# Performance work log

Hardware: AMD Instinct MI355X
Metric: run time of the kernel (lower is better)

The kernel has to match this reference:

```python
import jax, jax.numpy as jnp
import numpy as np

H = 256; NH = 4; DH = H // NH
NT, NS, NV = 4096, 2048, 1024
E1, E2, E3 = 65536, 16384, 32768
LN_EPS = 1e-5


def setup_inputs() -> dict:
    key = jax.random.key(0)
    ks = jax.random.split(key, 40)
    def nrm(i, shape):
        return jax.random.normal(ks[i], shape, jnp.float32) * 0.05
    inp = {
        "x_term": jax.random.normal(ks[0], (NT, H), jnp.float32),
        "x_symbol": jax.random.normal(ks[1], (NS, H), jnp.float32),
        "x_var": jax.random.normal(ks[2], (NV, H), jnp.float32),
        "ha_src": jax.random.randint(ks[3], (E1,), 0, NT),
        "ha_dst": jax.random.randint(ks[4], (E1,), 0, NT),
        "so_src": jax.random.randint(ks[5], (E2,), 0, NT),
        "so_dst": jax.random.randint(ks[6], (E2,), 0, NS),
        "vo_src": jax.random.randint(ks[7], (E3,), 0, NV),
        "vo_dst": jax.random.randint(ks[8], (E3,), 0, NT),
        # SAGEConv params for the 4 term-destination relations
        "Wl_rha": nrm(9, (H, H)),  "bl_rha": nrm(10, (H,)), "Wr_rha": nrm(11, (H, H)),
        "Wl_ha":  nrm(12, (H, H)), "bl_ha":  nrm(13, (H,)), "Wr_ha":  nrm(14, (H, H)),
        "Wl_rsym": nrm(15, (H, H)), "bl_rsym": nrm(16, (H,)), "Wr_rsym": nrm(17, (H, H)),
        "Wl_var": nrm(18, (H, H)), "bl_var": nrm(19, (H,)), "Wr_var": nrm(20, (H, H)),
        "ln_g": jnp.ones((H,), jnp.float32),
        "ln_b": jnp.zeros((H,), jnp.float32),
        "in_proj_w": nrm(21, (3 * H, H)),
        "in_proj_b": nrm(22, (3 * H,)),
        "out_proj_w": nrm(23, (H, H)),
        "out_proj_b": nrm(24, (H,)),
        "post_w": nrm(25, (H, H)),
        "post_b": nrm(26, (H,)),
    }
    return inp


def _sage(x_src, x_dst, src, dst, Wl, bl, Wr, num_dst):
    # PyG SAGEConv: lin_l(mean_j x_src[j]) + lin_r(x_dst)
    msg = x_src[src]                                            # [E, H] gather
    s = jax.ops.segment_sum(msg, dst, num_segments=num_dst)     # [N_dst, H] scatter-add
    cnt = jax.ops.segment_sum(jnp.ones((src.shape[0],), x_src.dtype), dst,
                              num_segments=num_dst)
    agg = s / jnp.maximum(cnt, 1.0)[:, None]
    return agg @ Wl.T + bl + x_dst @ Wr.T


def _layernorm(x, g, b):
    mu = jnp.mean(x, axis=-1, keepdims=True)
    var = jnp.mean(jnp.square(x - mu), axis=-1, keepdims=True)
    return (x - mu) * jax.lax.rsqrt(var + LN_EPS) * g + b


def _mha(x, in_w, in_b, out_w, out_b):
    # torch MultiheadAttention (eval, batch=1, self-attention)
    qkv = x @ in_w.T + in_b                       # [N, 3H]
    q, k, v = jnp.split(qkv, 3, axis=-1)
    def heads(t):
        return t.reshape(-1, NH, DH).transpose(1, 0, 2)  # [NH, N, DH]
    q, k, v = heads(q), heads(k), heads(v)
    scores = jnp.einsum("hqd,hkd->hqk", q, k) / np.sqrt(DH).astype(np.float32)
    a = jax.nn.softmax(scores, axis=-1)
    o = jnp.einsum("hqk,hkd->hqd", a, v)          # [NH, N, DH]
    o = o.transpose(1, 0, 2).reshape(-1, H)
    return o @ out_w.T + out_b


def reference(x_term, x_symbol, x_var,
              ha_src, ha_dst, so_src, so_dst, vo_src, vo_dst,
              Wl_rha, bl_rha, Wr_rha, Wl_ha, bl_ha, Wr_ha,
              Wl_rsym, bl_rsym, Wr_rsym, Wl_var, bl_var, Wr_var,
              ln_g, ln_b, in_proj_w, in_proj_b, out_proj_w, out_proj_b,
              post_w, post_b):
    nt = x_term.shape[0]
    # HeteroConv(aggr='sum') over the 4 relations whose destination is 'term'
    conv_term = (
        _sage(x_term, x_term, ha_dst, ha_src, Wl_rha, bl_rha, Wr_rha, nt)    # rev_has_arg
        + _sage(x_term, x_term, ha_src, ha_dst, Wl_ha, bl_ha, Wr_ha, nt)     # has_arg
        + _sage(x_symbol, x_term, so_dst, so_src, Wl_rsym, bl_rsym, Wr_rsym, nt)  # rev_symbol_of
        + _sage(x_var, x_term, vo_src, vo_dst, Wl_var, bl_var, Wr_var, nt)   # var_occurrence
    )
    term_out = _layernorm(conv_term + x_term, ln_g, ln_b)  # dropout is identity in eval
    attn_out = _mha(term_out, in_proj_w, in_proj_b, out_proj_w, out_proj_b)
    post = jax.nn.relu(attn_out @ post_w.T + post_b)
    term_final = post + term_out
    return term_final
```

## Files before the change

kernel.cpp:

```cpp
#include <hip/hip_runtime.h>
#include <hip/hip_bf16.h>

#define H 256
#define NT 4096
#define NHEAD 4
#define E1 65536
#define E2 16384
#define E3 32768
#define TOTE (2 * E1 + E2 + E3)
#define LN_EPS 1e-5f
#define SPLIT 4

typedef __hip_bfloat16 bf16;
typedef short bf16x8 __attribute__((ext_vector_type(8)));
typedef float f32x4 __attribute__((ext_vector_type(4)));

__device__ __forceinline__ float b2f(bf16 v) { return __bfloat162float(v); }
__device__ __forceinline__ float u2f(unsigned short u) {
    unsigned int x = ((unsigned int)u) << 16;
    return __uint_as_float(x);
}
__device__ __forceinline__ unsigned short f2u(float f) {
    bf16 h = __float2bfloat16(f);
    unsigned short v;
    __builtin_memcpy(&v, &h, 2);
    return v;
}
__device__ __forceinline__ float ldin(const void* p, size_t i, bool isbf) {
    return isbf ? b2f(((const bf16*)p)[i]) : ((const float*)p)[i];
}
__device__ __forceinline__ void gload_lds16(const void* g, void* l) {
    __builtin_amdgcn_global_load_lds(
        (const __attribute__((address_space(1))) unsigned int*)g,
        (__attribute__((address_space(3))) unsigned int*)l, 16, 0, 0);
}

__global__ __launch_bounds__(256) void k_init(float4* cnt4, int n4,
                                              const unsigned int* __restrict__ lng,
                                              unsigned int* __restrict__ flag) {
    int i = blockIdx.x * 256 + threadIdx.x;
    if (i == 0) *flag = (lng[0] == 0x3F803F80u) ? 1u : 0u;
    int stride = gridDim.x * 256;
    float4 z = make_float4(0.f, 0.f, 0.f, 0.f);
    for (; i < n4; i += stride) cnt4[i] = z;
}

__global__ __launch_bounds__(256) void k_count4(const int* __restrict__ s0, const int* __restrict__ s1,
                                                const int* __restrict__ s2, const int* __restrict__ s3,
                                                int* __restrict__ cnt) {
    int i = blockIdx.x * 256 + threadIdx.x;
    int r, e;
    if (i < E1) { r = 0; e = i; }
    else if (i < 2 * E1) { r = 1; e = i - E1; }
    else if (i < 2 * E1 + E2) { r = 2; e = i - 2 * E1; }
    else if (i < TOTE) { r = 3; e = i - 2 * E1 - E2; }
    else return;
    const int* s = (r == 0) ? s0 : (r == 1) ? s1 : (r == 2) ? s2 : s3;
    atomicAdd(&cnt[r * NT + s[e]], 1);
}

__global__ __launch_bounds__(256) void k_scan(const int* __restrict__ cnt, int* __restrict__ offs,
                                              int* __restrict__ cursor) {
    __shared__ int tot[256];
    int t = threadIdx.x, r = blockIdx.x;
    const int* c = cnt + r * NT;
    int* o = offs + r * (NT + 1);
    int* cur = cursor + r * NT;
    int base = t * 16;
    int local[16];
    int sum = 0;
#pragma unroll
    for (int j = 0; j < 16; j++) { local[j] = c[base + j]; sum += local[j]; }
    tot[t] = sum;
    __syncthreads();
    if (t == 0) {
        int run = 0;
        for (int i = 0; i < 256; i++) { int v = tot[i]; tot[i] = run; run += v; }
        o[NT] = run;
    }
    __syncthreads();
    int run = tot[t];
#pragma unroll
    for (int j = 0; j < 16; j++) { o[base + j] = run; cur[base + j] = run; run += local[j]; }
}

__global__ __launch_bounds__(256) void k_fill(const int* __restrict__ s0, const int* __restrict__ s1,
                                              const int* __restrict__ s2, const int* __restrict__ s3,
                                              const int* __restrict__ g0, const int* __restrict__ g1,
                                              const int* __restrict__ g2, const int* __restrict__ g3,
                                              int* __restrict__ cursor, int* __restrict__ csr) {
    int i = blockIdx.x * 256 + threadIdx.x;
    int r, e, rb;
    if (i < E1) { r = 0; e = i; rb = 0; }
    else if (i < 2 * E1) { r = 1; e = i - E1; rb = E1; }
    else if (i < 2 * E1 + E2) { r = 2; e = i - 2 * E1; rb = 2 * E1; }
    else if (i < TOTE) { r = 3; e = i - 2 * E1 - E2; rb = 2 * E1 + E2; }
    else return;
    const int* s = (r == 0) ? s0 : (r == 1) ? s1 : (r == 2) ? s2 : s3;
    const int* g = (r == 0) ? g0 : (r == 1) ? g1 : (r == 2) ? g2 : g3;
    int d = s[e];
    int pos = atomicAdd(&cursor[r * NT + d], 1);
    csr[rb + pos] = g[e];
}

__global__ __launch_bounds__(256) void k_gatherA(
    const void* __restrict__ x0, const void* __restrict__ x1,
    const void* __restrict__ x2, const void* __restrict__ x3,
    const int* __restrict__ offs, const int* __restrict__ csr,
    bf16* __restrict__ aggs, const unsigned int* __restrict__ flag) {
    int y = blockIdx.y;
    int i = blockIdx.x * 4 + (threadIdx.x >> 6);
    int lane = threadIdx.x & 63;
    bool isbf = (*flag != 0u);
    const void* x = (y == 0) ? x0 : (y == 1) ? x1 : (y == 2) ? x2 : x3;
    static const int rbase[4] = {0, E1, 2 * E1, 2 * E1 + E2};
    const int* o = offs + y * (NT + 1);
    const int* cs = csr + rbase[y];
    int b = o[i], e = o[i + 1];
    float ax = 0.f, ay = 0.f, az = 0.f, aw = 0.f;
    if (isbf) {
        for (int j = b; j < e; j++) {
            int s = cs[j];
            ushort4 u = *(const ushort4*)((const unsigned short*)x + (size_t)s * H + lane * 4);
            ax += u2f(u.x); ay += u2f(u.y); az += u2f(u.z); aw += u2f(u.w);
        }
    } else {
        for (int j = b; j < e; j++) {
            int s = cs[j];
            float4 v = *(const float4*)((const float*)x + (size_t)s * H + lane * 4);
            ax += v.x; ay += v.y; az += v.z; aw += v.w;
        }
    }
    float inv = 1.0f / fmaxf((float)(e - b), 1.0f);
    *(ushort4*)((unsigned short*)aggs + ((size_t)y * NT + i) * H + lane * 4) =
        make_ushort4(f2u(ax * inv), f2u(ay * inv), f2u(az * inv), f2u(aw * inv));
}

__global__ __launch_bounds__(256) void k_prepB(
    const void* __restrict__ Wl0, const void* __restrict__ Wl1,
    const void* __restrict__ Wl2, const void* __restrict__ Wl3,
    const void* __restrict__ Wr0, const void* __restrict__ Wr1,
    const void* __restrict__ Wr2, const void* __restrict__ Wr3,
    const void* __restrict__ b0, const void* __restrict__ b1,
    const void* __restrict__ b2, const void* __restrict__ b3,
    bf16* __restrict__ Bcat, float* __restrict__ bsum, const unsigned int* __restrict__ flag) {
    int idx = blockIdx.x * 256 + threadIdx.x;
    bool isbf = (*flag != 0u);
    int n = idx / 1280, k = idx % 1280;
    float v;
    if (k < 1024) {
        const void* W = (k < 256) ? Wl0 : (k < 512) ? Wl1 : (k < 768) ? Wl2 : Wl3;
        v = ldin(W, (size_t)n * 256 + (k & 255), isbf);
    } else {
        size_t o = (size_t)n * 256 + (k - 1024);
        v = ldin(Wr0, o, isbf) + ldin(Wr1, o, isbf) + ldin(Wr2, o, isbf) + ldin(Wr3, o, isbf);
    }
    ((unsigned short*)Bcat)[idx] = f2u(v);
    if (idx < 256)
        bsum[idx] = ldin(b0, idx, isbf) + ldin(b1, idx, isbf) + ldin(b2, idx, isbf) + ldin(b3, idx, isbf);
}

__global__ __launch_bounds__(256) void k_convln(
    const bf16* __restrict__ aggs, const bf16* __restrict__ Bcat, const float* __restrict__ bsum,
    const void* __restrict__ xt, const void* __restrict__ gw, const void* __restrict__ gb,
    bf16* __restrict__ term, const unsigned int* __restrict__ flag) {
    __shared__ unsigned short Asm[8 * 16 * 8];
    __shared__ unsigned short Bsm[8 * 256 * 8];
    __shared__ float redS[4][16];
    const bool isbf = (*flag != 0u);
    const int tid = threadIdx.x;
    const int w = tid >> 6, lane = tid & 63;
    const int col = lane & 15, quad = lane >> 4;
    const int m0 = blockIdx.x * 16;
    const int srow = tid & 63, skq = tid >> 6;

    f32x4 acc[4];
#pragma unroll
    for (int dt = 0; dt < 4; dt++) acc[dt] = (f32x4){0.f, 0.f, 0.f, 0.f};

    bf16x8 areg;
    bf16x8 breg[8];
    auto loadA = [&](int k0) {
        if (tid < 128) {
            int row = tid & 15, akq = tid >> 4;
            int k = k0 + akq * 8;
            if (k < 1024) {
                areg = *(const bf16x8*)((const unsigned short*)aggs +
                                        ((size_t)(k >> 8) * NT + m0 + row) * 256 + (k & 255));
            } else {
#pragma unroll
                for (int j = 0; j < 8; j++)
                    areg[j] = (short)f2u(ldin(xt, (size_t)(m0 + row) * 256 + (k - 1024) + j, isbf));
            }
        }
    };
    auto loadB = [&](int k0) {
#pragma unroll
        for (int t = 0; t < 4; t++)
#pragma unroll
            for (int kk = 0; kk < 2; kk++)
                breg[t * 2 + kk] = *(const bf16x8*)((const unsigned short*)Bcat +
                                       (size_t)(t * 64 + srow) * 1280 + k0 + (skq * 2 + kk) * 8);
    };

    loadA(0);
    loadB(0);
    for (int k0 = 0; k0 < 1280; k0 += 64) {
        __syncthreads();
        if (tid < 128) *(bf16x8*)&Asm[tid * 8] = areg;
#pragma unroll
        for (int t = 0; t < 4; t++)
#pragma unroll
            for (int kk = 0; kk < 2; kk++)
                *(bf16x8*)&Bsm[((skq * 2 + kk) * 256 + t * 64 + srow) * 8] = breg[t * 2 + kk];
        __syncthreads();
        if (k0 + 64 < 1280) { loadA(k0 + 64); loadB(k0 + 64); }
#pragma unroll
        for (int ch = 0; ch < 2; ch++) {
            bf16x8 a = *(const bf16x8*)&Asm[(((ch * 4 + quad) & 7) * 16 + col) * 8];
#pragma unroll
            for (int dt = 0; dt < 4; dt++) {
                bf16x8 b = *(const bf16x8*)&Bsm[((ch * 4 + quad) * 256 + w * 64 + dt * 16 + col) * 8];
                acc[dt] = __builtin_amdgcn_mfma_f32_16x16x32_bf16(a, b, acc[dt], 0, 0, 0);
            }
        }
    }

#pragma unroll
    for (int dt = 0; dt < 4; dt++) {
        int n = w * 64 + dt * 16 + col;
        float bsv = bsum[n];
#pragma unroll
        for (int r = 0; r < 4; r++) {
            int m = m0 + quad * 4 + r;
            acc[dt][r] += bsv + ldin(xt, (size_t)m * 256 + n, isbf);
        }
    }
    float mu[4], rs_[4];
#pragma unroll
    for (int r = 0; r < 4; r++) {
        float s = acc[0][r] + acc[1][r] + acc[2][r] + acc[3][r];
#pragma unroll
        for (int mk = 1; mk <= 8; mk <<= 1) s += __shfl_xor(s, mk);
        if (col == 0) redS[w][quad * 4 + r] = s;
    }
    __syncthreads();
#pragma unroll
    for (int r = 0; r < 4; r++) {
        int m = quad * 4 + r;
        mu[r] = (redS[0][m] + redS[1][m] + redS[2][m] + redS[3][m]) * (1.0f / 256.0f);
    }
    __syncthreads();
#pragma unroll
    for (int r = 0; r < 4; r++) {
        float s2 = 0.f;
#pragma unroll
        for (int dt = 0; dt < 4; dt++) {
            float d = acc[dt][r] - mu[r];
            s2 += d * d;
        }
#pragma unroll
        for (int mk = 1; mk <= 8; mk <<= 1) s2 += __shfl_xor(s2, mk);
        if (col == 0) redS[w][quad * 4 + r] = s2;
    }
    __syncthreads();
#pragma unroll
    for (int r = 0; r < 4; r++) {
        int m = quad * 4 + r;
        float var = (redS[0][m] + redS[1][m] + redS[2][m] + redS[3][m]) * (1.0f / 256.0f);
        rs_[r] = rsqrtf(var + LN_EPS);
    }
#pragma unroll
    for (int dt = 0; dt < 4; dt++) {
        int n = w * 64 + dt * 16 + col;
        float gv = ldin(gw, n, isbf), bv = ldin(gb, n, isbf);
#pragma unroll
        for (int r = 0; r < 4; r++) {
            int m = m0 + quad * 4 + r;
            term[(size_t)m * 256 + n] = __float2bfloat16((acc[dt][r] - mu[r]) * rs_[r] * gv + bv);
        }
    }
}

template <int AMODE, int EPI>
__global__ __launch_bounds__(256) void k_gemm(
    const void* __restrict__ A, const void* __restrict__ A2, const float* __restrict__ ml,
    const void* __restrict__ B, const void* __restrict__ bias,
    const bf16* __restrict__ resid, bf16* __restrict__ vt, void* __restrict__ outp,
    int M, int N, int K, const unsigned int* __restrict__ flag) {
    __shared__ unsigned short Asm[8 * 64 * 8];
    __shared__ unsigned short Bsm[8 * 64 * 8];
    const bool isbf = (*flag != 0u);
    const int tid = threadIdx.x;
    const int w = tid >> 6, lane = tid & 63;
    const int col = lane & 15, quad = lane >> 4;
    const int m0 = blockIdx.x * 64, n0 = blockIdx.y * 64;
    const int srow = tid & 63, skq = tid >> 6;
    const int am = m0 + srow;

    f32x4 acc[4];
#pragma unroll
    for (int dt = 0; dt < 4; dt++) acc[dt] = (f32x4){0.f, 0.f, 0.f, 0.f};

    bf16x8 areg[2], breg[2];
    auto loadA = [&](int k0) {
#pragma unroll
        for (int c = 0; c < 2; c++) {
            int k = k0 + skq * 16 + c * 8;
            if (AMODE == 0) {
                areg[c] = *(const bf16x8*)((const unsigned short*)A + (size_t)am * K + k);
            } else {
                int h = k >> 6;
                float l0 = ml[(size_t)(0 * NHEAD + h) * NT + am];
                float l1 = ml[(size_t)(1 * NHEAD + h) * NT + am];
                float l2 = ml[(size_t)(2 * NHEAD + h) * NT + am];
                float l3 = ml[(size_t)(3 * NHEAD + h) * NT + am];
                float iw = 1.0f / (l0 + l1 + l2 + l3);
                bf16x8 o0 = *(const bf16x8*)((const unsigned short*)A + (size_t)am * H + k);
                bf16x8 o1 = *(const bf16x8*)((const unsigned short*)A + ((size_t)NT + am) * H + k);
                bf16x8 o2 = *(const bf16x8*)((const unsigned short*)A2 + (size_t)am * H + k);
                bf16x8 o3 = *(const bf16x8*)((const unsigned short*)A2 + ((size_t)NT + am) * H + k);
#pragma unroll
                for (int j = 0; j < 8; j++)
                    areg[c][j] = (short)f2u((l0 * u2f((unsigned short)o0[j]) + l1 * u2f((unsigned short)o1[j]) +
                                             l2 * u2f((unsigned short)o2[j]) + l3 * u2f((unsigned short)o3[j])) * iw);
            }
        }
    };
    auto loadB = [&](int k0) {
#pragma unroll
        for (int c = 0; c < 2; c++) {
            size_t bi = (size_t)(n0 + srow) * K + k0 + skq * 16 + c * 8;
            if (isbf) {
                breg[c] = *(const bf16x8*)((const unsigned short*)B + bi);
            } else {
#pragma unroll
                for (int j = 0; j < 8; j++) breg[c][j] = (short)f2u(((const float*)B)[bi + j]);
            }
        }
    };

    loadA(0);
    loadB(0);
    for (int k0 = 0; k0 < K; k0 += 64) {
        __syncthreads();
#pragma unroll
        for (int c = 0; c < 2; c++) {
            *(bf16x8*)&Asm[((skq * 2 + c) * 64 + srow) * 8] = areg[c];
            *(bf16x8*)&Bsm[((skq * 2 + c) * 64 + srow) * 8] = breg[c];
        }
        __syncthreads();
        if (k0 + 64 < K) { loadA(k0 + 64); loadB(k0 + 64); }
#pragma unroll
        for (int ch = 0; ch < 2; ch++) {
            bf16x8 a = *(const bf16x8*)&Asm[((ch * 4 + quad) * 64 + w * 16 + col) * 8];
#pragma unroll
            for (int dt = 0; dt < 4; dt++) {
                bf16x8 b = *(const bf16x8*)&Bsm[((ch * 4 + quad) * 64 + dt * 16 + col) * 8];
                acc[dt] = __builtin_amdgcn_mfma_f32_16x16x32_bf16(a, b, acc[dt], 0, 0, 0);
            }
        }
    }
#pragma unroll
    for (int dt = 0; dt < 4; dt++) {
        int n = n0 + dt * 16 + col;
        float bv = ldin(bias, n, isbf);
        if (EPI == 3 && n0 >= 512) {
            int m = m0 + w * 16 + quad * 4;
            *(ushort4*)((unsigned short*)vt + (size_t)(n - 512) * NT + m) =
                make_ushort4(f2u(acc[dt][0] + bv), f2u(acc[dt][1] + bv),
                             f2u(acc[dt][2] + bv), f2u(acc[dt][3] + bv));
            continue;
        }
#pragma unroll
        for (int r = 0; r < 4; r++) {
            int m = m0 + w * 16 + quad * 4 + r;
            float v = acc[dt][r] + bv;
            if (EPI == 3) {
                ((bf16*)outp)[(size_t)m * 512 + n] = __float2bfloat16(v);
            } else if (EPI == 2) {
                size_t off = (size_t)m * N + n;
                v = fmaxf(v, 0.f);
                v += b2f(resid[off]);
                ((float*)outp)[off] = v;
            } else {
                ((bf16*)outp)[(size_t)m * N + n] = __float2bfloat16(v);
            }
        }
    }
}

__global__ __launch_bounds__(256) void k_attn(const bf16* __restrict__ qkvQK,
                                              const bf16* __restrict__ vt,
                                              bf16* __restrict__ opart01,
                                              bf16* __restrict__ opart23,
                                              float* __restrict__ ml) {
    __shared__ unsigned short Ksm[2][8 * 64 * 8];
    __shared__ unsigned short Vsm[2][8 * 64 * 8];
    const int h = blockIdx.y, sp = blockIdx.z;
    const int q0 = blockIdx.x * 64;
    const int tid = threadIdx.x;
    const int w = tid >> 6, lane = tid & 63;
    const int col = lane & 15, quad = lane >> 4;
    const unsigned short* qk = (const unsigned short*)qkvQK;
    const unsigned short* vp = (const unsigned short*)vt;

    bf16x8 aQ[2];
#pragma unroll
    for (int ch = 0; ch < 2; ch++)
        aQ[ch] = *(const bf16x8*)(qk + (size_t)(q0 + w * 16 + col) * 512 +
                                  h * 64 + ch * 32 + quad * 8);

    f32x4 O[4];
#pragma unroll
    for (int dt = 0; dt < 4; dt++) O[dt] = (f32x4){0.f, 0.f, 0.f, 0.f};
    float lsum = 0.f;

    const int kbeg = sp * (NT / SPLIT), kend = kbeg + NT / SPLIT;
    const float SC = 0.125f * 1.44269504f;

    auto stage = [&](int kb, int buf) {
#pragma unroll
        for (int it = 0; it < 2; it++) {
            int dhq = it * 4 + w;
            gload_lds16(qk + (size_t)(kb + lane) * 512 + 256 + h * 64 + dhq * 8,
                        &Ksm[buf][(it * 256 + w * 64) * 8]);
            gload_lds16(vp + (size_t)(h * 64 + lane) * NT + kb + dhq * 8,
                        &Vsm[buf][(it * 256 + w * 64) * 8]);
        }
    };

    stage(kbeg, 0);
    stage(kbeg + 64, 1);
    for (int kb = kbeg; kb < kend; kb += 64) {
        const int cur = ((kb - kbeg) >> 6) & 1;
        if (kb + 64 < kend) {
            asm volatile("s_waitcnt vmcnt(4)" ::: "memory");
        } else {
            asm volatile("s_waitcnt vmcnt(0)" ::: "memory");
        }
        __builtin_amdgcn_s_barrier();
        __builtin_amdgcn_sched_barrier(0);

        f32x4 c[4];
        __builtin_amdgcn_s_setprio(1);
#pragma unroll
        for (int dt = 0; dt < 4; dt++) {
            c[dt] = (f32x4){0.f, 0.f, 0.f, 0.f};
#pragma unroll
            for (int ch = 0; ch < 2; ch++) {
                bf16x8 kf = *(const bf16x8*)&Ksm[cur][((ch * 4 + quad) * 64 + dt * 16 + col) * 8];
                c[dt] = __builtin_amdgcn_mfma_f32_16x16x32_bf16(kf, aQ[ch], c[dt], 0, 0, 0);
            }
        }
        __builtin_amdgcn_s_setprio(0);

        float pp[4][4];
#pragma unroll
        for (int dt = 0; dt < 4; dt++) {
#pragma unroll
            for (int r = 0; r < 4; r++) {
                pp[dt][r] = __builtin_amdgcn_exp2f(c[dt][r] * SC);
            }
            lsum += (pp[dt][0] + pp[dt][1]) + (pp[dt][2] + pp[dt][3]);
        }

        union PU { unsigned int u[4]; bf16x8 v; };
        PU ap[2];
#pragma unroll
        for (int kc = 0; kc < 2; kc++) {
            unsigned int a0, a1, b0, b1;
            asm("v_cvt_pk_bf16_f32 %0, %1, %2" : "=v"(a0) : "v"(pp[2 * kc][0]), "v"(pp[2 * kc][1]));
            asm("v_cvt_pk_bf16_f32 %0, %1, %2" : "=v"(a1) : "v"(pp[2 * kc][2]), "v"(pp[2 * kc][3]));
            asm("v_cvt_pk_bf16_f32 %0, %1, %2" : "=v"(b0) : "v"(pp[2 * kc + 1][0]), "v"(pp[2 * kc + 1][1]));
            asm("v_cvt_pk_bf16_f32 %0, %1, %2" : "=v"(b1) : "v"(pp[2 * kc + 1][2]), "v"(pp[2 * kc + 1][3]));
            asm("v_permlane32_swap_b32 %0, %1" : "+v"(a0), "+v"(b0));
            asm("v_permlane16_swap_b32 %0, %1" : "+v"(a0), "+v"(b0));
            asm("v_permlane32_swap_b32 %0, %1" : "+v"(a1), "+v"(b1));
            asm("v_permlane16_swap_b32 %0, %1" : "+v"(a1), "+v"(b1));
            ap[kc].u[0] = a0; ap[kc].u[1] = a1; ap[kc].u[2] = b0; ap[kc].u[3] = b1;
        }

        __builtin_amdgcn_s_setprio(1);
#pragma unroll
        for (int dt = 0; dt < 4; dt++)
#pragma unroll
            for (int kc = 0; kc < 2; kc++) {
                bf16x8 b = *(const bf16x8*)&Vsm[cur][((kc * 4 + quad) * 64 + dt * 16 + col) * 8];
                O[dt] = __builtin_amdgcn_mfma_f32_16x16x32_bf16(ap[kc].v, b, O[dt], 0, 0, 0);
            }
        __builtin_amdgcn_s_setprio(0);

        __builtin_amdgcn_sched_barrier(0);
        __builtin_amdgcn_s_barrier();
        if (kb + 128 < kend) stage(kb + 128, cur);
    }
    float l = lsum;
    l += __shfl_xor(l, 16);
    l += __shfl_xor(l, 32);
    bf16* ob = (sp < 2) ? (opart01 + (size_t)sp * NT * H) : (opart23 + (size_t)(sp - 2) * NT * H);
    if (quad == 0)
        ml[((size_t)sp * NHEAD + h) * NT + (q0 + w * 16 + col)] = l;
    float lr[4];
#pragma unroll
    for (int r = 0; r < 4; r++) lr[r] = __shfl(l, quad * 4 + r, 16);
#pragma unroll
    for (int dt = 0; dt < 4; dt++) {
#pragma unroll
        for (int r = 0; r < 4; r++) {
            int q = q0 + w * 16 + quad * 4 + r;
            ob[(size_t)q * H + h * 64 + dt * 16 + col] = __float2bfloat16(O[dt][r] / lr[r]);
        }
    }
}

extern "C" void kernel_launch(void* const* d_in, const int* in_sizes, int n_in,
                              void* d_out, int out_size, void* d_ws, size_t ws_size,
                              hipStream_t stream) {
    const void* x_term   = d_in[0];
    const void* x_symbol = d_in[1];
    const void* x_var    = d_in[2];
    const int* ha_src = (const int*)d_in[3];
    const int* ha_dst = (const int*)d_in[4];
    const int* so_src = (const int*)d_in[5];
    const int* so_dst = (const int*)d_in[6];
    const int* vo_src = (const int*)d_in[7];
    const int* vo_dst = (const int*)d_in[8];
    const void* Wl[4]  = {d_in[9],  d_in[12], d_in[15], d_in[18]};
    const void* blv[4] = {d_in[10], d_in[13], d_in[16], d_in[19]};
    const void* Wr[4]  = {d_in[11], d_in[14], d_in[17], d_in[20]};
    const void* ln_g = d_in[21];
    const void* ln_b = d_in[22];
    const void* in_w = d_in[23];
    const void* in_b = d_in[24];
    const void* out_w = d_in[25];
    const void* out_b = d_in[26];
    const void* post_w = d_in[27];
    const void* post_b = d_in[28];

    char* ws = (char*)d_ws;
    unsigned int* flag = (unsigned int*)ws;
    char* csrbase = ws + 256;
    int* cnt    = (int*)csrbase;
    int* offs   = (int*)(csrbase + 65536);
    int* cursor = (int*)(csrbase + 132096);
    int* csr    = (int*)(csrbase + 197632);
    bf16*  Bcat = (bf16*)csrbase;
    float* bsum = (float*)(csrbase + 655360);
    float* ml   = (float*)csrbase;
    bf16* aggs  = (bf16*)(ws + (1 << 20));
    bf16* term  = (bf16*)(ws + (1 << 20) + 8388608);
    bf16* opart23 = (bf16*)(ws + (1 << 20) + 10485760);
    bf16* qkvQK = aggs;
    bf16* vt    = (bf16*)((char*)aggs + 4194304);
    bf16* proj  = aggs;
    bf16* opart01 = (bf16*)d_out;

    k_init<<<16, 256, 0, stream>>>((float4*)cnt, 4 * NT / 4, (const unsigned int*)ln_g, flag);
    k_count4<<<(TOTE + 255) / 256, 256, 0, stream>>>(ha_src, ha_dst, so_src, vo_dst, cnt);
    k_scan<<<4, 256, 0, stream>>>(cnt, offs, cursor);
    k_fill<<<(TOTE + 255) / 256, 256, 0, stream>>>(ha_src, ha_dst, so_src, vo_dst,
                                                   ha_dst, ha_src, so_dst, vo_src, cursor, csr);
    k_gatherA<<<dim3(NT / 4, 4), 256, 0, stream>>>(x_term, x_term, x_symbol, x_var,
                                                   offs, csr, aggs, flag);
    k_prepB<<<(256 * 1280) / 256, 256, 0, stream>>>(Wl[0], Wl[1], Wl[2], Wl[3],
                                                    Wr[0], Wr[1], Wr[2], Wr[3],
                                                    blv[0], blv[1], blv[2], blv[3],
                                                    Bcat, bsum, flag);

    k_convln<<<256, 256, 0, stream>>>(aggs, Bcat, bsum, x_term, ln_g, ln_b, term, flag);

    k_gemm<0, 3><<<dim3(64, 12), 256, 0, stream>>>(
        term, nullptr, nullptr, in_w, in_b, nullptr, vt, qkvQK, NT, 768, 256, flag);

    k_attn<<<dim3(64, NHEAD, SPLIT), 256, 0, stream>>>(qkvQK, vt, opart01, opart23, ml);

    k_gemm<1, 0><<<dim3(64, 4), 256, 0, stream>>>(
        opart01, opart23, ml, out_w, out_b, nullptr, nullptr, proj, NT, 256, 256, flag);

    k_gemm<0, 2><<<dim3(64, 4), 256, 0, stream>>>(
        proj, nullptr, nullptr, post_w, post_b, term, nullptr, d_out, NT, 256, 256, flag);

    (void)in_sizes; (void)n_in; (void)out_size; (void)ws_size;
}
```

Baseline: 275.9 us.

## Load full K=256 tiles once in GEMM, unroll gather by two, drop init kernel

The GEMM now stages the entire K=256 A and B tiles into LDS in one go, using direct global-to-LDS loads where possible, and runs all MFMAs after a single barrier. This replaces the register-pipelined 64-wide K loop and its repeated barriers. The gather loop is unrolled by two with independent accumulators to keep more row loads in flight. The init kernel is replaced by hipMemsetAsync, with the dtype flag now set in k_scan. The larger LDS footprint (64 KB per block) can cut occupancy, and loading everything up front removes any overlap between loads and compute.

Result: no change. 273.8 us (-0.8%).

```diff
diff --git a/kernel.cpp b/kernel.cpp
--- a/kernel.cpp
+++ b/kernel.cpp
@@ -33,16 +33,6 @@
     __builtin_amdgcn_global_load_lds(
         (const __attribute__((address_space(1))) unsigned int*)g,
         (__attribute__((address_space(3))) unsigned int*)l, 16, 0, 0);
-}
-
-__global__ __launch_bounds__(256) void k_init(float4* cnt4, int n4,
-                                              const unsigned int* __restrict__ lng,
-                                              unsigned int* __restrict__ flag) {
-    int i = blockIdx.x * 256 + threadIdx.x;
-    if (i == 0) *flag = (lng[0] == 0x3F803F80u) ? 1u : 0u;
-    int stride = gridDim.x * 256;
-    float4 z = make_float4(0.f, 0.f, 0.f, 0.f);
-    for (; i < n4; i += stride) cnt4[i] = z;
 }
 
 __global__ __launch_bounds__(256) void k_count4(const int* __restrict__ s0, const int* __restrict__ s1,
@@ -60,9 +50,12 @@
 }
 
 __global__ __launch_bounds__(256) void k_scan(const int* __restrict__ cnt, int* __restrict__ offs,
-                                              int* __restrict__ cursor) {
+                                              int* __restrict__ cursor,
+                                              const unsigned int* __restrict__ lng,
+                                              unsigned int* __restrict__ flag) {
     __shared__ int tot[256];
     int t = threadIdx.x, r = blockIdx.x;
+    if (r == 0 && t == 0) *flag = (lng[0] == 0x3F803F80u) ? 1u : 0u;
     const int* c = cnt + r * NT;
     int* o = offs + r * (NT + 1);
     int* cur = cursor + r * NT;
@@ -118,19 +111,36 @@
     const int* cs = csr + rbase[y];
     int b = o[i], e = o[i + 1];
     float ax = 0.f, ay = 0.f, az = 0.f, aw = 0.f;
+    float bx = 0.f, by = 0.f, bz = 0.f, bw = 0.f;
+    int j = b;
     if (isbf) {
-        for (int j = b; j < e; j++) {
+        for (; j + 2 <= e; j += 2) {
+            int s0 = cs[j], s1 = cs[j + 1];
+            ushort4 u0 = *(const ushort4*)((const unsigned short*)x + (size_t)s0 * H + lane * 4);
+            ushort4 u1 = *(const ushort4*)((const unsigned short*)x + (size_t)s1 * H + lane * 4);
+            ax += u2f(u0.x); ay += u2f(u0.y); az += u2f(u0.z); aw += u2f(u0.w);
+            bx += u2f(u1.x); by += u2f(u1.y); bz += u2f(u1.z); bw += u2f(u1.w);
+        }
+        if (j < e) {
             int s = cs[j];
             ushort4 u = *(const ushort4*)((const unsigned short*)x + (size_t)s * H + lane * 4);
             ax += u2f(u.x); ay += u2f(u.y); az += u2f(u.z); aw += u2f(u.w);
         }
     } else {
-        for (int j = b; j < e; j++) {
+        for (; j + 2 <= e; j += 2) {
+            int s0 = cs[j], s1 = cs[j + 1];
+            float4 v0 = *(const float4*)((const float*)x + (size_t)s0 * H + lane * 4);
+            float4 v1 = *(const float4*)((const float*)x + (size_t)s1 * H + lane * 4);
+            ax += v0.x; ay += v0.y; az += v0.z; aw += v0.w;
+            bx += v1.x; by += v1.y; bz += v1.z; bw += v1.w;
+        }
+        if (j < e) {
             int s = cs[j];
             float4 v = *(const float4*)((const float*)x + (size_t)s * H + lane * 4);
             ax += v.x; ay += v.y; az += v.z; aw += v.w;
         }
     }
+    ax += bx; ay += by; az += bz; aw += bw;
     float inv = 1.0f / fmaxf((float)(e - b), 1.0f);
     *(ushort4*)((unsigned short*)aggs + ((size_t)y * NT + i) * H + lane * 4) =
         make_ushort4(f2u(ax * inv), f2u(ay * inv), f2u(az * inv), f2u(aw * inv));
@@ -288,8 +298,8 @@
     const void* __restrict__ B, const void* __restrict__ bias,
     const bf16* __restrict__ resid, bf16* __restrict__ vt, void* __restrict__ outp,
     int M, int N, int K, const unsigned int* __restrict__ flag) {
-    __shared__ unsigned short Asm[8 * 64 * 8];
-    __shared__ unsigned short Bsm[8 * 64 * 8];
+    __shared__ unsigned short Asm[32 * 64 * 8];
+    __shared__ unsigned short Bsm[32 * 64 * 8];
     const bool isbf = (*flag != 0u);
     const int tid = threadIdx.x;
     const int w = tid >> 6, lane = tid & 63;
@@ -298,67 +308,61 @@
     const int srow = tid & 63, skq = tid >> 6;
     const int am = m0 + srow;
 
+    if (AMODE == 0) {
+#pragma unroll
+        for (int c = 0; c < 8; c++) {
+            gload_lds16((const unsigned short*)A + (size_t)(m0 + lane) * K + skq * 64 + c * 8,
+                        &Asm[((skq * 8 + c) * 64) * 8]);
+        }
+    } else {
+        float l0 = ml[(size_t)(0 * NHEAD + skq) * NT + am];
+        float l1 = ml[(size_t)(1 * NHEAD + skq) * NT + am];
+        float l2 = ml[(size_t)(2 * NHEAD + skq) * NT + am];
+        float l3 = ml[(size_t)(3 * NHEAD + skq) * NT + am];
+        float iw = 1.0f / (l0 + l1 + l2 + l3);
+#pragma unroll
+        for (int c = 0; c < 8; c++) {
+            int k = skq * 64 + c * 8;
+            bf16x8 o0 = *(const bf16x8*)((const unsigned short*)A + (size_t)am * H + k);
+            bf16x8 o1 = *(const bf16x8*)((const unsigned short*)A + ((size_t)NT + am) * H + k);
+            bf16x8 o2 = *(const bf16x8*)((const unsigned short*)A2 + (size_t)am * H + k);
+            bf16x8 o3 = *(const bf16x8*)((const unsigned short*)A2 + ((size_t)NT + am) * H + k);
+            bf16x8 areg;
+#pragma unroll
+            for (int j = 0; j < 8; j++)
+                areg[j] = (short)f2u((l0 * u2f((unsigned short)o0[j]) + l1 * u2f((unsigned short)o1[j]) +
+                                      l2 * u2f((unsigned short)o2[j]) + l3 * u2f((unsigned short)o3[j])) * iw);
+            *(bf16x8*)&Asm[((skq * 8 + c) * 64 + srow) * 8] = areg;
+        }
+    }
+    if (isbf) {
+#pragma unroll
+        for (int c = 0; c < 8; c++) {
+            gload_lds16((const unsigned short*)B + (size_t)(n0 + lane) * K + skq * 64 + c * 8,
+                        &Bsm[((skq * 8 + c) * 64) * 8]);
+        }
+    } else {
+#pragma unroll
+        for (int c = 0; c < 8; c++) {
+            size_t bi = (size_t)(n0 + srow) * K + skq * 64 + c * 8;
+            bf16x8 breg;
+#pragma unroll
+            for (int j = 0; j < 8; j++) breg[j] = (short)f2u(((const float*)B)[bi + j]);
+            *(bf16x8*)&Bsm[((skq * 8 + c) * 64 + srow) * 8] = breg;
+        }
+    }
+    __syncthreads();
+
     f32x4 acc[4];
 #pragma unroll
     for (int dt = 0; dt < 4; dt++) acc[dt] = (f32x4){0.f, 0.f, 0.f, 0.f};
-
-    bf16x8 areg[2], breg[2];
-    auto loadA = [&](int k0) {
-#pragma unroll
-        for (int c = 0; c < 2; c++) {
-            int k = k0 + skq * 16 + c * 8;
-            if (AMODE == 0) {
-                areg[c] = *(const bf16x8*)((const unsigned short*)A + (size_t)am * K + k);
-            } else {
-                int h = k >> 6;
-                float l0 = ml[(size_t)(0 * NHEAD + h) * NT + am];
-                float l1 = ml[(size_t)(1 * NHEAD + h) * NT + am];
-                float l2 = ml[(size_t)(2 * NHEAD + h) * NT + am];
-                float l3 = ml[(size_t)(3 * NHEAD + h) * NT + am];
-                float iw = 1.0f / (l0 + l1 + l2 + l3);
-                bf16x8 o0 = *(const bf16x8*)((const unsigned short*)A + (size_t)am * H + k);
-                bf16x8 o1 = *(const bf16x8*)((const unsigned short*)A + ((size_t)NT + am) * H + k);
-                bf16x8 o2 = *(const bf16x8*)((const unsigned short*)A2 + (size_t)am * H + k);
-                bf16x8 o3 = *(const bf16x8*)((const unsigned short*)A2 + ((size_t)NT + am) * H + k);
-#pragma unroll
-                for (int j = 0; j < 8; j++)
-                    areg[c][j] = (short)f2u((l0 * u2f((unsigned short)o0[j]) + l1 * u2f((unsigned short)o1[j]) +
-                                             l2 * u2f((unsigned short)o2[j]) + l3 * u2f((unsigned short)o3[j])) * iw);
-            }
-        }
-    };
-    auto loadB = [&](int k0) {
-#pragma unroll
-        for (int c = 0; c < 2; c++) {
-            size_t bi = (size_t)(n0 + srow) * K + k0 + skq * 16 + c * 8;
-            if (isbf) {
-                breg[c] = *(const bf16x8*)((const unsigned short*)B + bi);
-            } else {
-#pragma unroll
-                for (int j = 0; j < 8; j++) breg[c][j] = (short)f2u(((const float*)B)[bi + j]);
-            }
-        }
-    };
-
-    loadA(0);
-    loadB(0);
-    for (int k0 = 0; k0 < K; k0 += 64) {
-        __syncthreads();
-#pragma unroll
-        for (int c = 0; c < 2; c++) {
-            *(bf16x8*)&Asm[((skq * 2 + c) * 64 + srow) * 8] = areg[c];
-            *(bf16x8*)&Bsm[((skq * 2 + c) * 64 + srow) * 8] = breg[c];
-        }
-        __syncthreads();
-        if (k0 + 64 < K) { loadA(k0 + 64); loadB(k0 + 64); }
-#pragma unroll
-        for (int ch = 0; ch < 2; ch++) {
-            bf16x8 a = *(const bf16x8*)&Asm[((ch * 4 + quad) * 64 + w * 16 + col) * 8];
-#pragma unroll
-            for (int dt = 0; dt < 4; dt++) {
-                bf16x8 b = *(const bf16x8*)&Bsm[((ch * 4 + quad) * 64 + dt * 16 + col) * 8];
-                acc[dt] = __builtin_amdgcn_mfma_f32_16x16x32_bf16(a, b, acc[dt], 0, 0, 0);
-            }
+#pragma unroll
+    for (int kk = 0; kk < 8; kk++) {
+        bf16x8 a = *(const bf16x8*)&Asm[((kk * 4 + quad) * 64 + w * 16 + col) * 8];
+#pragma unroll
+        for (int dt = 0; dt < 4; dt++) {
+            bf16x8 b = *(const bf16x8*)&Bsm[((kk * 4 + quad) * 64 + dt * 16 + col) * 8];
+            acc[dt] = __builtin_amdgcn_mfma_f32_16x16x32_bf16(a, b, acc[dt], 0, 0, 0);
         }
     }
 #pragma unroll
@@ -388,6 +392,7 @@
             }
         }
     }
+    (void)M;
 }
 
 __global__ __launch_bounds__(256) void k_attn(const bf16* __restrict__ qkvQK,
@@ -556,9 +561,9 @@
     bf16* proj  = aggs;
     bf16* opart01 = (bf16*)d_out;
 
-    k_init<<<16, 256, 0, stream>>>((float4*)cnt, 4 * NT / 4, (const unsigned int*)ln_g, flag);
+    hipMemsetAsync(cnt, 0, 4 * NT * sizeof(int), stream);
     k_count4<<<(TOTE + 255) / 256, 256, 0, stream>>>(ha_src, ha_dst, so_src, vo_dst, cnt);
-    k_scan<<<4, 256, 0, stream>>>(cnt, offs, cursor);
+    k_scan<<<4, 256, 0, stream>>>(cnt, offs, cursor, (const unsigned int*)ln_g, flag);
     k_fill<<<(TOTE + 255) / 256, 256, 0, stream>>>(ha_src, ha_dst, so_src, vo_dst,
                                                    ha_dst, ha_src, so_dst, vo_src, cursor, csr);
     k_gatherA<<<dim3(NT / 4, 4), 256, 0, stream>>>(x_term, x_term, x_symbol, x_var,
```
